# Kernel tuning notes

Hardware: AMD Instinct MI355X
Metric: run time of the kernel (lower is better)

Reference implementation:

```python
import jax, jax.numpy as jnp
import numpy as np

C, PH, PW, H, W = 10, 7, 7, 34, 34
STRIDE = 16.0  # heat_map_a
S = 4          # sample_per_part
P = PH * PW


def setup_inputs() -> dict:
    key = jax.random.key(0)
    k1, k2, k3, k4, k5 = jax.random.split(key, 5)
    N = 16384
    ft = jax.random.normal(k1, (1, C * PH * PW, H, W), dtype=jnp.float32)
    x1 = jax.random.uniform(k2, (N,), minval=0.0, maxval=400.0)
    y1 = jax.random.uniform(k3, (N,), minval=0.0, maxval=400.0)
    bw = jax.random.uniform(k4, (N,), minval=8.0, maxval=200.0)
    bh = jax.random.uniform(k5, (N,), minval=8.0, maxval=200.0)
    rois = jnp.stack([jnp.zeros((N,), jnp.float32), x1, y1, x1 + bw, y1 + bh], axis=1)
    return {"ft_add_left_right": ft, "rois": rois}


def _forward(ft_all, rois):
    ft = ft_all[0].reshape(C, PH, PW, H, W)
    roi_start_w = rois[:, 1] / STRIDE
    roi_start_h = rois[:, 2] / STRIDE
    roi_end_w = rois[:, 3] / STRIDE
    roi_end_h = rois[:, 4] / STRIDE
    roi_h = roi_end_h - roi_start_h
    roi_w = roi_end_w - roi_start_w
    # torch.threshold(x, 0.1, 0.1): keep x where x > 0.1 else 0.1
    roi_h = jnp.where(roi_h > 0.1, roi_h, 0.1)
    roi_w = jnp.where(roi_w > 0.1, roi_w, 0.1)
    bin_h = roi_h / PH
    bin_w = roi_w / PW
    sub_h = bin_h / S
    sub_w = bin_w / S
    gh, gw = jnp.meshgrid(jnp.arange(PH), jnp.arange(PW), indexing="ij")
    phs = gh.reshape(-1, 1)  # (P,1)
    pws = gw.reshape(-1, 1)
    hstart = jnp.floor(roi_start_h + phs * bin_h)  # (P,N)
    wstart = jnp.floor(roi_start_w + pws * bin_w)

    offs = jnp.asarray([[ih, iw] for ih in range(S) for iw in range(S)], dtype=jnp.float32)

    def gather(y, x):  # y,x: (P,N) int32 -> (C,P,N)
        return ft[:, phs, pws, y, x]

    def body(carry, off):
        sum_, count = carry
        w = wstart + (off[1] + 0.5) * sub_w  # (P,N)
        h = hstart + (off[0] + 0.5) * sub_h
        keep = (w > -1) & (w < W) & (h > -1) & (h < H)
        x1f = jnp.floor(w); x2f = jnp.ceil(w)
        y1f = jnp.floor(h); y2f = jnp.ceil(h)
        x1v = ((x1f >= 0) & (x1f < W)).astype(jnp.float32)
        x2v = ((x2f >= 0) & (x2f < W)).astype(jnp.float32)
        y1v = ((y1f >= 0) & (y1f < H)).astype(jnp.float32)
        y2v = ((y2f >= 0) & (y2f < H)).astype(jnp.float32)
        x1 = jnp.clip(x1f, 0, W - 1).astype(jnp.int32)
        x2 = jnp.clip(x2f, 0, W - 1).astype(jnp.int32)
        y1 = jnp.clip(y1f, 0, H - 1).astype(jnp.int32)
        y2 = jnp.clip(y2f, 0, H - 1).astype(jnp.int32)
        dx = w - x1.astype(jnp.float32)
        dy = h - y1.astype(jnp.float32)
        v11 = gather(y1, x1) * (x1v * y1v)
        v12 = gather(y2, x1) * (x1v * y2v)
        v21 = gather(y1, x2) * (x2v * y1v)
        v22 = gather(y2, x2) * (x2v * y2v)
        value = ((1 - dx) * (1 - dy) * v11 + (1 - dx) * dy * v12
                 + dx * (1 - dy) * v21 + dx * dy * v22)
        kf = keep.astype(jnp.float32)
        return (sum_ + value * kf, count + kf), None

    N = rois.shape[0]
    init = (jnp.zeros((C, P, N), jnp.float32), jnp.zeros((P, N), jnp.float32))
    (sum_, count), _ = jax.lax.scan(body, init, offs)
    out = sum_ / jnp.where(count > 0, count, 1.0)
    return out.transpose(2, 0, 1)  # (N, C, P)


def reference(ft_add_left_right, rois):
    return _forward(ft_add_left_right, rois)
```

## Files before the change

kernel.cpp:

```cpp
#include <hip/hip_runtime.h>


constexpr int C  = 10;
constexpr int PH = 7;
constexpr int PW = 7;
constexpr int H  = 34;
constexpr int W  = 34;
constexpr int P  = PH * PW;
constexpr int HW = H * W;
constexpr int FT_C_STRIDE = P * HW;
constexpr int CP = 12;
constexpr int R  = C * P;

template <bool COALESCED>
__global__ __launch_bounds__(512, 4) void dfmb_phase1(
    const float* __restrict__ ft,
    const float* __restrict__ rois,
    float* __restrict__ dst,
    int N)
{
    __shared__ float tile[HW * CP];

    const int p  = blockIdx.y;
    const int ph = p / PW;
    const int pw = p - ph * PW;

    const float* __restrict__ src = ft + p * HW;
    for (int i = threadIdx.x; i < C * HW; i += 512) {
        int c = i / HW;
        int r = i - c * HW;
        tile[r * CP + c] = src[c * FT_C_STRIDE + r];
    }
    __syncthreads();

    const int n = blockIdx.x * 512 + threadIdx.x;
    if (n >= N) return;

    float wstart, hstart, sub_w, sub_h;
    {
#pragma clang fp contract(off)
        const float inv_stride = 0.0625f;
        float rsw = rois[n * 5 + 1] * inv_stride;
        float rsh = rois[n * 5 + 2] * inv_stride;
        float rew = rois[n * 5 + 3] * inv_stride;
        float reh = rois[n * 5 + 4] * inv_stride;
        float roi_h = reh - rsh; if (!(roi_h > 0.1f)) roi_h = 0.1f;
        float roi_w = rew - rsw; if (!(roi_w > 0.1f)) roi_w = 0.1f;
        float bin_h = roi_h / 7.0f;
        float bin_w = roi_w / 7.0f;
        sub_h = bin_h * 0.25f;
        sub_w = bin_w * 0.25f;
        hstart = floorf(rsh + (float)ph * bin_h);
        wstart = floorf(rsw + (float)pw * bin_w);
    }

    float Xw0 = 0.f, Xw1 = 0.f, Xw2 = 0.f, Xw3 = 0.f, cntx = 0.f;
    int xbase = 0;
#pragma unroll
    for (int iw = 0; iw < 4; ++iw) {
        float w;
        {
#pragma clang fp contract(off)
            w = wstart + ((float)iw + 0.5f) * sub_w;
        }
        float kw  = (w > -1.0f && w < 34.0f) ? 1.0f : 0.0f;
        float x1f = floorf(w), x2f = ceilf(w);
        float x1v = (x1f >= 0.0f && x1f < 34.0f) ? 1.0f : 0.0f;
        float x2v = (x2f >= 0.0f && x2f < 34.0f) ? 1.0f : 0.0f;
        int x1 = (int)fminf(fmaxf(x1f, 0.0f), 33.0f);
        int x2 = (int)fminf(fmaxf(x2f, 0.0f), 33.0f);
        float dx = w - (float)x1;
        if (iw == 0) xbase = x1;
        float a = kw * (1.0f - dx) * x1v;
        float b = kw * dx * x2v;
        int i1 = x1 - xbase, i2 = x2 - xbase;
        Xw0 += (i1 == 0) ? a : 0.f;  Xw1 += (i1 == 1) ? a : 0.f;
        Xw2 += (i1 == 2) ? a : 0.f;  Xw3 += (i1 == 3) ? a : 0.f;
        Xw0 += (i2 == 0) ? b : 0.f;  Xw1 += (i2 == 1) ? b : 0.f;
        Xw2 += (i2 == 2) ? b : 0.f;  Xw3 += (i2 == 3) ? b : 0.f;
        cntx += kw;
    }

    float Yw0 = 0.f, Yw1 = 0.f, Yw2 = 0.f, Yw3 = 0.f, cnty = 0.f;
    int ybase = 0;
#pragma unroll
    for (int ih = 0; ih < 4; ++ih) {
        float h;
        {
#pragma clang fp contract(off)
            h = hstart + ((float)ih + 0.5f) * sub_h;
        }
        float kh  = (h > -1.0f && h < 34.0f) ? 1.0f : 0.0f;
        float y1f = floorf(h), y2f = ceilf(h);
        float y1v = (y1f >= 0.0f && y1f < 34.0f) ? 1.0f : 0.0f;
        float y2v = (y2f >= 0.0f && y2f < 34.0f) ? 1.0f : 0.0f;
        int y1 = (int)fminf(fmaxf(y1f, 0.0f), 33.0f);
        int y2 = (int)fminf(fmaxf(y2f, 0.0f), 33.0f);
        float dy = h - (float)y1;
        if (ih == 0) ybase = y1;
        float a = kh * (1.0f - dy) * y1v;
        float b = kh * dy * y2v;
        int i1 = y1 - ybase, i2 = y2 - ybase;
        Yw0 += (i1 == 0) ? a : 0.f;  Yw1 += (i1 == 1) ? a : 0.f;
        Yw2 += (i1 == 2) ? a : 0.f;  Yw3 += (i1 == 3) ? a : 0.f;
        Yw0 += (i2 == 0) ? b : 0.f;  Yw1 += (i2 == 1) ? b : 0.f;
        Yw2 += (i2 == 2) ? b : 0.f;  Yw3 += (i2 == 3) ? b : 0.f;
        cnty += kh;
    }

    float4 s0 = {0.f, 0.f, 0.f, 0.f};
    float4 s1 = {0.f, 0.f, 0.f, 0.f};
    float2 s2 = {0.f, 0.f};
#pragma unroll
    for (int cy = 0; cy < 4; ++cy) {
        float wy = (cy == 0) ? Yw0 : (cy == 1) ? Yw1 : (cy == 2) ? Yw2 : Yw3;
        if (wy != 0.0f) {
            int yy = min(ybase + cy, 33);
            const float* rowp = &tile[yy * (W * CP)];
#pragma unroll
            for (int cx = 0; cx < 4; ++cx) {
                float wx = (cx == 0) ? Xw0 : (cx == 1) ? Xw1
                         : (cx == 2) ? Xw2 : Xw3;
                float wgt = wy * wx;
                if (wgt != 0.0f) {
                    int xx = min(xbase + cx, 33);
                    const float* t = rowp + xx * CP;
                    float4 v0 = *(const float4*)(t);
                    float4 v1 = *(const float4*)(t + 4);
                    float2 v2 = *(const float2*)(t + 8);
                    s0.x += wgt * v0.x; s0.y += wgt * v0.y;
                    s0.z += wgt * v0.z; s0.w += wgt * v0.w;
                    s1.x += wgt * v1.x; s1.y += wgt * v1.y;
                    s1.z += wgt * v1.z; s1.w += wgt * v1.w;
                    s2.x += wgt * v2.x; s2.y += wgt * v2.y;
                }
            }
        }
    }

    float cnt = cntx * cnty;
    if (!(cnt > 0.0f)) cnt = 1.0f;
    float inv = 1.0f / cnt;
    float r[10] = { s0.x * inv, s0.y * inv, s0.z * inv, s0.w * inv,
                    s1.x * inv, s1.y * inv, s1.z * inv, s1.w * inv,
                    s2.x * inv, s2.y * inv };

    if (COALESCED) {
        float* __restrict__ o = dst + (size_t)(n >> 6) * (R * 64)
                                    + (size_t)p * 64 + (n & 63);
#pragma unroll
        for (int c = 0; c < C; ++c) o[(size_t)(c * P) * 64] = r[c];
    } else {
        float* __restrict__ o = dst + (size_t)n * R + p;
#pragma unroll
        for (int c = 0; c < C; ++c) o[c * P] = r[c];
    }
}

constexpr int TR = 245;
__global__ __launch_bounds__(1024) void dfmb_phase2(
    const float* __restrict__ ws, float* __restrict__ out, int N)
{
    __shared__ float t[TR * 65];
    const int nblk = blockIdx.x;
    const int r0   = blockIdx.y * TR;
    const float* __restrict__ srcb = ws + (size_t)nblk * (R * 64) + (size_t)r0 * 64;

    for (int i = threadIdx.x; i < TR * 16; i += 1024) {
        int rr  = i >> 4;
        int nl4 = (i & 15) * 4;
        float4 v = ((const float4*)srcb)[i];
        float* tp = &t[rr * 65 + nl4];
        tp[0] = v.x; tp[1] = v.y; tp[2] = v.z; tp[3] = v.w;
    }
    __syncthreads();

    const int n0 = nblk * 64;
    for (int i = threadIdx.x; i < 64 * TR; i += 1024) {
        int nl = i / TR;
        int r  = i - nl * TR;
        out[(size_t)(n0 + nl) * R + r0 + r] = t[r * 65 + nl];
    }
}

extern "C" void kernel_launch(void* const* d_in, const int* in_sizes, int n_in,
                              void* d_out, int out_size, void* d_ws, size_t ws_size,
                              hipStream_t stream) {
    const float* ft   = (const float*)d_in[0];
    const float* rois = (const float*)d_in[1];
    float* out = (float*)d_out;
    const int N = in_sizes[1] / 5;

    dim3 grid1((N + 511) / 512, P);
    const size_t need = (size_t)R * N * sizeof(float);
    if (d_ws != nullptr && ws_size >= need && (N % 64) == 0) {
        float* ws = (float*)d_ws;
        dfmb_phase1<true><<<grid1, dim3(512), 0, stream>>>(ft, rois, ws, N);
        dim3 grid2(N / 64, 2);
        dfmb_phase2<<<grid2, dim3(1024), 0, stream>>>(ws, out, N);
    } else {
        dfmb_phase1<false><<<grid1, dim3(512), 0, stream>>>(ft, rois, out, N);
    }
}
```

Baseline: 110.4 us.

## Fuse transpose into sampling kernel via pre-swizzled feature map and LDS output staging

Adds a small swizzle kernel that rewrites the feature map into a channel-interleaved layout (12 floats per pixel) in workspace. A single fused kernel then handles 16 ROIs across all 49 parts per block, reading features straight from global/L2 and staging its output in shared memory so it can write contiguous float4 rows to the final layout. This removes the intermediate workspace write/read and the separate transpose kernel, trading LDS-resident tiles for global gathers that depend on L2 hit rates. The fallback path is simplified to direct uncoalesced writes.

```diff
diff --git a/kernel.cpp b/kernel.cpp
--- a/kernel.cpp
+++ b/kernel.cpp
@@ -11,20 +11,172 @@
 constexpr int FT_C_STRIDE = P * HW;
 constexpr int CP = 12;
 constexpr int R  = C * P;
-
-template <bool COALESCED>
-__global__ __launch_bounds__(512, 4) void dfmb_phase1(
+constexpr int NB = 16;
+
+__global__ __launch_bounds__(256) void dfmb_swizzle(
+    const float* __restrict__ ft, float* __restrict__ ftT)
+{
+    const int p = blockIdx.x;
+    const int c = blockIdx.y;
+    const float* __restrict__ src = ft + (size_t)c * FT_C_STRIDE + p * HW;
+    float* __restrict__ dst = ftT + (size_t)p * (HW * CP) + c;
+    for (int pix = threadIdx.x; pix < HW; pix += 256)
+        dst[(size_t)pix * CP] = src[pix];
+}
+
+__global__ __launch_bounds__(256, 4) void dfmb_fused(
+    const float* __restrict__ ftT,
+    const float* __restrict__ rois,
+    float* __restrict__ out,
+    int N)
+{
+    __shared__ float olds[NB * R];
+
+    const int n0 = blockIdx.x * NB;
+
+    for (int k = 0; k < 4; ++k) {
+        const int j = threadIdx.x + k * 256;
+        if (j < P * NB) {
+            const int p     = j >> 4;
+            const int n_loc = j & 15;
+            const int n     = n0 + n_loc;
+            const int ph = p / PW;
+            const int pw = p - ph * PW;
+
+            float wstart, hstart, sub_w, sub_h;
+            {
+#pragma clang fp contract(off)
+                const float inv_stride = 0.0625f;
+                float rsw = rois[n * 5 + 1] * inv_stride;
+                float rsh = rois[n * 5 + 2] * inv_stride;
+                float rew = rois[n * 5 + 3] * inv_stride;
+                float reh = rois[n * 5 + 4] * inv_stride;
+                float roi_h = reh - rsh; if (!(roi_h > 0.1f)) roi_h = 0.1f;
+                float roi_w = rew - rsw; if (!(roi_w > 0.1f)) roi_w = 0.1f;
+                float bin_h = roi_h / 7.0f;
+                float bin_w = roi_w / 7.0f;
+                sub_h = bin_h * 0.25f;
+                sub_w = bin_w * 0.25f;
+                hstart = floorf(rsh + (float)ph * bin_h);
+                wstart = floorf(rsw + (float)pw * bin_w);
+            }
+
+            float Xw0 = 0.f, Xw1 = 0.f, Xw2 = 0.f, Xw3 = 0.f, cntx = 0.f;
+            int xbase = 0;
+#pragma unroll
+            for (int iw = 0; iw < 4; ++iw) {
+                float w;
+                {
+#pragma clang fp contract(off)
+                    w = wstart + ((float)iw + 0.5f) * sub_w;
+                }
+                float kw  = (w > -1.0f && w < 34.0f) ? 1.0f : 0.0f;
+                float x1f = floorf(w), x2f = ceilf(w);
+                float x1v = (x1f >= 0.0f && x1f < 34.0f) ? 1.0f : 0.0f;
+                float x2v = (x2f >= 0.0f && x2f < 34.0f) ? 1.0f : 0.0f;
+                int x1 = (int)fminf(fmaxf(x1f, 0.0f), 33.0f);
+                int x2 = (int)fminf(fmaxf(x2f, 0.0f), 33.0f);
+                float dx = w - (float)x1;
+                if (iw == 0) xbase = x1;
+                float a = kw * (1.0f - dx) * x1v;
+                float b = kw * dx * x2v;
+                int i1 = x1 - xbase, i2 = x2 - xbase;
+                Xw0 += (i1 == 0) ? a : 0.f;  Xw1 += (i1 == 1) ? a : 0.f;
+                Xw2 += (i1 == 2) ? a : 0.f;  Xw3 += (i1 == 3) ? a : 0.f;
+                Xw0 += (i2 == 0) ? b : 0.f;  Xw1 += (i2 == 1) ? b : 0.f;
+                Xw2 += (i2 == 2) ? b : 0.f;  Xw3 += (i2 == 3) ? b : 0.f;
+                cntx += kw;
+            }
+
+            float Yw0 = 0.f, Yw1 = 0.f, Yw2 = 0.f, Yw3 = 0.f, cnty = 0.f;
+            int ybase = 0;
+#pragma unroll
+            for (int ih = 0; ih < 4; ++ih) {
+                float h;
+                {
+#pragma clang fp contract(off)
+                    h = hstart + ((float)ih + 0.5f) * sub_h;
+                }
+                float kh  = (h > -1.0f && h < 34.0f) ? 1.0f : 0.0f;
+                float y1f = floorf(h), y2f = ceilf(h);
+                float y1v = (y1f >= 0.0f && y1f < 34.0f) ? 1.0f : 0.0f;
+                float y2v = (y2f >= 0.0f && y2f < 34.0f) ? 1.0f : 0.0f;
+                int y1 = (int)fminf(fmaxf(y1f, 0.0f), 33.0f);
+                int y2 = (int)fminf(fmaxf(y2f, 0.0f), 33.0f);
+                float dy = h - (float)y1;
+                if (ih == 0) ybase = y1;
+                float a = kh * (1.0f - dy) * y1v;
+                float b = kh * dy * y2v;
+                int i1 = y1 - ybase, i2 = y2 - ybase;
+                Yw0 += (i1 == 0) ? a : 0.f;  Yw1 += (i1 == 1) ? a : 0.f;
+                Yw2 += (i1 == 2) ? a : 0.f;  Yw3 += (i1 == 3) ? a : 0.f;
+                Yw0 += (i2 == 0) ? b : 0.f;  Yw1 += (i2 == 1) ? b : 0.f;
+                Yw2 += (i2 == 2) ? b : 0.f;  Yw3 += (i2 == 3) ? b : 0.f;
+                cnty += kh;
+            }
+
+            const float* __restrict__ slab = ftT + (size_t)p * (HW * CP);
+            float4 s0 = {0.f, 0.f, 0.f, 0.f};
+            float4 s1 = {0.f, 0.f, 0.f, 0.f};
+            float2 s2 = {0.f, 0.f};
+#pragma unroll
+            for (int cy = 0; cy < 4; ++cy) {
+                float wy = (cy == 0) ? Yw0 : (cy == 1) ? Yw1 : (cy == 2) ? Yw2 : Yw3;
+                if (wy != 0.0f) {
+                    int yy = min(ybase + cy, 33);
+                    const float* rowp = slab + yy * (W * CP);
+#pragma unroll
+                    for (int cx = 0; cx < 4; ++cx) {
+                        float wx = (cx == 0) ? Xw0 : (cx == 1) ? Xw1
+                                 : (cx == 2) ? Xw2 : Xw3;
+                        float wgt = wy * wx;
+                        if (wgt != 0.0f) {
+                            int xx = min(xbase + cx, 33);
+                            const float* t = rowp + xx * CP;
+                            float4 v0 = *(const float4*)(t);
+                            float4 v1 = *(const float4*)(t + 4);
+                            float2 v2 = *(const float2*)(t + 8);
+                            s0.x += wgt * v0.x; s0.y += wgt * v0.y;
+                            s0.z += wgt * v0.z; s0.w += wgt * v0.w;
+                            s1.x += wgt * v1.x; s1.y += wgt * v1.y;
+                            s1.z += wgt * v1.z; s1.w += wgt * v1.w;
+                            s2.x += wgt * v2.x; s2.y += wgt * v2.y;
+                        }
+                    }
+                }
+            }
+
+            float cnt = cntx * cnty;
+            if (!(cnt > 0.0f)) cnt = 1.0f;
+            float inv = 1.0f / cnt;
+
+            float* __restrict__ ol = olds + n_loc * R + p;
+            ol[0 * P] = s0.x * inv;  ol[1 * P] = s0.y * inv;
+            ol[2 * P] = s0.z * inv;  ol[3 * P] = s0.w * inv;
+            ol[4 * P] = s1.x * inv;  ol[5 * P] = s1.y * inv;
+            ol[6 * P] = s1.z * inv;  ol[7 * P] = s1.w * inv;
+            ol[8 * P] = s2.x * inv;  ol[9 * P] = s2.y * inv;
+        }
+    }
+
+    __syncthreads();
+
+    float4* __restrict__ dst4 = (float4*)(out + (size_t)n0 * R);
+    const float4* __restrict__ src4 = (const float4*)olds;
+    for (int i = threadIdx.x; i < (NB * R) / 4; i += 256)
+        dst4[i] = src4[i];
+}
+
+__global__ __launch_bounds__(512, 4) void dfmb_phase1_direct(
     const float* __restrict__ ft,
     const float* __restrict__ rois,
     float* __restrict__ dst,
     int N)
 {
     __shared__ float tile[HW * CP];
-
     const int p  = blockIdx.y;
     const int ph = p / PW;
     const int pw = p - ph * PW;
-
     const float* __restrict__ src = ft + p * HW;
     for (int i = threadIdx.x; i < C * HW; i += 512) {
         int c = i / HW;
@@ -32,10 +184,8 @@
         tile[r * CP + c] = src[c * FT_C_STRIDE + r];
     }
     __syncthreads();
-
     const int n = blockIdx.x * 512 + threadIdx.x;
     if (n >= N) return;
-
     float wstart, hstart, sub_w, sub_h;
     {
 #pragma clang fp contract(off)
@@ -53,9 +203,9 @@
         hstart = floorf(rsh + (float)ph * bin_h);
         wstart = floorf(rsw + (float)pw * bin_w);
     }
-
-    float Xw0 = 0.f, Xw1 = 0.f, Xw2 = 0.f, Xw3 = 0.f, cntx = 0.f;
-    int xbase = 0;
+    float Xw[4] = {0,0,0,0}, Yw[4] = {0,0,0,0};
+    float cntx = 0.f, cnty = 0.f;
+    int xbase = 0, ybase = 0;
 #pragma unroll
     for (int iw = 0; iw < 4; ++iw) {
         float w;
@@ -71,18 +221,10 @@
         int x2 = (int)fminf(fmaxf(x2f, 0.0f), 33.0f);
         float dx = w - (float)x1;
         if (iw == 0) xbase = x1;
-        float a = kw * (1.0f - dx) * x1v;
-        float b = kw * dx * x2v;
-        int i1 = x1 - xbase, i2 = x2 - xbase;
-        Xw0 += (i1 == 0) ? a : 0.f;  Xw1 += (i1 == 1) ? a : 0.f;
-        Xw2 += (i1 == 2) ? a : 0.f;  Xw3 += (i1 == 3) ? a : 0.f;
-        Xw0 += (i2 == 0) ? b : 0.f;  Xw1 += (i2 == 1) ? b : 0.f;
-        Xw2 += (i2 == 2) ? b : 0.f;  Xw3 += (i2 == 3) ? b : 0.f;
+        Xw[x1 - xbase] += kw * (1.0f - dx) * x1v;
+        Xw[x2 - xbase] += kw * dx * x2v;
         cntx += kw;
     }
-
-    float Yw0 = 0.f, Yw1 = 0.f, Yw2 = 0.f, Yw3 = 0.f, cnty = 0.f;
-    int ybase = 0;
 #pragma unroll
     for (int ih = 0; ih < 4; ++ih) {
         float h;
@@ -98,30 +240,20 @@
         int y2 = (int)fminf(fmaxf(y2f, 0.0f), 33.0f);
         float dy = h - (float)y1;
         if (ih == 0) ybase = y1;
-        float a = kh * (1.0f - dy) * y1v;
-        float b = kh * dy * y2v;
-        int i1 = y1 - ybase, i2 = y2 - ybase;
-        Yw0 += (i1 == 0) ? a : 0.f;  Yw1 += (i1 == 1) ? a : 0.f;
-        Yw2 += (i1 == 2) ? a : 0.f;  Yw3 += (i1 == 3) ? a : 0.f;
-        Yw0 += (i2 == 0) ? b : 0.f;  Yw1 += (i2 == 1) ? b : 0.f;
-        Yw2 += (i2 == 2) ? b : 0.f;  Yw3 += (i2 == 3) ? b : 0.f;
+        Yw[y1 - ybase] += kh * (1.0f - dy) * y1v;
+        Yw[y2 - ybase] += kh * dy * y2v;
         cnty += kh;
     }
-
-    float4 s0 = {0.f, 0.f, 0.f, 0.f};
-    float4 s1 = {0.f, 0.f, 0.f, 0.f};
-    float2 s2 = {0.f, 0.f};
+    float4 s0 = {0,0,0,0}, s1 = {0,0,0,0};
+    float2 s2 = {0,0};
 #pragma unroll
     for (int cy = 0; cy < 4; ++cy) {
-        float wy = (cy == 0) ? Yw0 : (cy == 1) ? Yw1 : (cy == 2) ? Yw2 : Yw3;
-        if (wy != 0.0f) {
+        if (Yw[cy] != 0.0f) {
             int yy = min(ybase + cy, 33);
             const float* rowp = &tile[yy * (W * CP)];
 #pragma unroll
             for (int cx = 0; cx < 4; ++cx) {
-                float wx = (cx == 0) ? Xw0 : (cx == 1) ? Xw1
-                         : (cx == 2) ? Xw2 : Xw3;
-                float wgt = wy * wx;
+                float wgt = Yw[cy] * Xw[cx];
                 if (wgt != 0.0f) {
                     int xx = min(xbase + cx, 33);
                     const float* t = rowp + xx * CP;
@@ -137,50 +269,15 @@
             }
         }
     }
-
     float cnt = cntx * cnty;
     if (!(cnt > 0.0f)) cnt = 1.0f;
     float inv = 1.0f / cnt;
-    float r[10] = { s0.x * inv, s0.y * inv, s0.z * inv, s0.w * inv,
-                    s1.x * inv, s1.y * inv, s1.z * inv, s1.w * inv,
-                    s2.x * inv, s2.y * inv };
-
-    if (COALESCED) {
-        float* __restrict__ o = dst + (size_t)(n >> 6) * (R * 64)
-                                    + (size_t)p * 64 + (n & 63);
-#pragma unroll
-        for (int c = 0; c < C; ++c) o[(size_t)(c * P) * 64] = r[c];
-    } else {
-        float* __restrict__ o = dst + (size_t)n * R + p;
-#pragma unroll
-        for (int c = 0; c < C; ++c) o[c * P] = r[c];
-    }
-}
-
-constexpr int TR = 245;
-__global__ __launch_bounds__(1024) void dfmb_phase2(
-    const float* __restrict__ ws, float* __restrict__ out, int N)
-{
-    __shared__ float t[TR * 65];
-    const int nblk = blockIdx.x;
-    const int r0   = blockIdx.y * TR;
-    const float* __restrict__ srcb = ws + (size_t)nblk * (R * 64) + (size_t)r0 * 64;
-
-    for (int i = threadIdx.x; i < TR * 16; i += 1024) {
-        int rr  = i >> 4;
-        int nl4 = (i & 15) * 4;
-        float4 v = ((const float4*)srcb)[i];
-        float* tp = &t[rr * 65 + nl4];
-        tp[0] = v.x; tp[1] = v.y; tp[2] = v.z; tp[3] = v.w;
-    }
-    __syncthreads();
-
-    const int n0 = nblk * 64;
-    for (int i = threadIdx.x; i < 64 * TR; i += 1024) {
-        int nl = i / TR;
-        int r  = i - nl * TR;
-        out[(size_t)(n0 + nl) * R + r0 + r] = t[r * 65 + nl];
-    }
+    float r[10] = { s0.x*inv, s0.y*inv, s0.z*inv, s0.w*inv,
+                    s1.x*inv, s1.y*inv, s1.z*inv, s1.w*inv,
+                    s2.x*inv, s2.y*inv };
+    float* __restrict__ o = dst + (size_t)n * R + p;
+#pragma unroll
+    for (int c = 0; c < C; ++c) o[c * P] = r[c];
 }
 
 extern "C" void kernel_launch(void* const* d_in, const int* in_sizes, int n_in,
@@ -191,14 +288,13 @@
     float* out = (float*)d_out;
     const int N = in_sizes[1] / 5;
 
-    dim3 grid1((N + 511) / 512, P);
-    const size_t need = (size_t)R * N * sizeof(float);
-    if (d_ws != nullptr && ws_size >= need && (N % 64) == 0) {
-        float* ws = (float*)d_ws;
-        dfmb_phase1<true><<<grid1, dim3(512), 0, stream>>>(ft, rois, ws, N);
-        dim3 grid2(N / 64, 2);
-        dfmb_phase2<<<grid2, dim3(1024), 0, stream>>>(ws, out, N);
+    const size_t need = (size_t)P * HW * CP * sizeof(float);
+    if (d_ws != nullptr && ws_size >= need && (N % NB) == 0) {
+        float* ftT = (float*)d_ws;
+        dfmb_swizzle<<<dim3(P, C), dim3(256), 0, stream>>>(ft, ftT);
+        dfmb_fused<<<dim3(N / NB), dim3(256), 0, stream>>>(ftT, rois, out, N);
     } else {
-        dfmb_phase1<false><<<grid1, dim3(512), 0, stream>>>(ft, rois, out, N);
+        dim3 grid1((N + 511) / 512, P);
+        dfmb_phase1_direct<<<grid1, dim3(512), 0, stream>>>(ft, rois, out, N);
     }
 }
```

New measurement: 103.7 us. 1.06x faster.
